# Optimization experiments

Measured on AMD Instinct MI355X. Metric: run time of the kernel, lower is better.

Reference implementation:

```python
import jax, jax.numpy as jnp
import numpy as np

B, F = 512, 300  # F must satisfy F+4 == 16*19
EPS = 1e-5

def _leaky(v):
    return jnp.where(v >= 0, v, 0.01 * v)

def setup_inputs() -> dict:
    key = jax.random.key(0)
    ks = jax.random.split(key, 9)
    def conv_w(k, o, i):
        return jax.random.normal(k, (o, i), dtype=jnp.float32) * (1.0 / np.sqrt(i))
    x = jax.random.uniform(ks[0], (B, F), dtype=jnp.float32)
    return {
        "x": x,
        "w1": conv_w(ks[1], 256, 512), "b1": jnp.zeros((256,), jnp.float32),
        "w2": conv_w(ks[2], 128, 256), "b2": jnp.zeros((128,), jnp.float32),
        "w3": conv_w(ks[3], 64, 128),  "b3": jnp.zeros((64,), jnp.float32),
        "w4": conv_w(ks[4], 4, 64),    "b4": jnp.zeros((4,), jnp.float32),
    }

def reference(x, w1, b1, w2, b2, w3, b3, w4, b4):
    b = x.shape[0]
    xp = jnp.pad(x, ((0, 0), (2, 2)))                       # (b, 304)
    s1 = xp[:, None, :]                                      # unsqueeze(1)
    s2 = xp[:, :, None]                                      # unsqueeze(2)
    DI = s1 - s2                                             # (b,304,304)
    NDI = DI / (s1 + s2 + EPS)
    t = jnp.stack([DI, NDI], axis=-1)                        # (b,304,304,2)
    # tile into 16x16 grid of 19x19 patches, concat patches along channel
    # channel c = (row*16+col)*2 + d  (row-major loop order in original)
    t = t.reshape(b, 16, 19, 16, 19, 2).transpose(0, 2, 4, 1, 3, 5).reshape(b, 19, 19, 512)
    h = _leaky(jnp.einsum('bhwc,oc->bhwo', t, w1) + b1)      # (b,19,19,256)
    h = _leaky(jnp.einsum('bhwc,oc->bhwo', h, w2) + b2)      # (b,19,19,128)
    # masking branch (positional encoding in original is dead code / overwritten)
    m = jax.nn.relu(jnp.einsum('bhwc,oc->bhwo', h, w3) + b3)  # (b,19,19,64)
    m = jax.nn.relu(jnp.einsum('bhwc,oc->bhwo', m, w4) + b4)  # (b,19,19,4)
    m = m.transpose(3, 0, 1, 2).reshape(4, b, 19 * 19)
    m = jax.nn.softmax(m, axis=2).reshape(4, b, 19, 19, 1)
    # split 128 channels into 4 groups of 32
    g = h.reshape(b, 19, 19, 4, 32).transpose(3, 0, 1, 2, 4)  # (4,b,19,19,32)
    out = (g * m).sum(axis=(2, 3))                            # (4,b,32)
    return out.transpose(1, 0, 2).reshape(b, 128)
```

## Files before the change

### kernel.cpp

```cpp
#include <hip/hip_runtime.h>
#include <math.h>

typedef unsigned short ushort_t;
typedef __attribute__((ext_vector_type(8))) short short8;
typedef __attribute__((ext_vector_type(4))) float f32x4;

#define NTILES 12

#define WS_W_USHORTS 115712

__device__ inline float bf2f(ushort_t h) { return __uint_as_float(((unsigned)h) << 16); }
__device__ inline ushort_t f2bf(float f) {
    unsigned u = __float_as_uint(f);
    return (ushort_t)((u + 0x7FFFu + ((u >> 16) & 1u)) >> 16);
}
__device__ inline unsigned pkbf(float f0, float f1) {
    unsigned a = __float_as_uint(f0) + 0x8000u;
    unsigned b = __float_as_uint(f1) + 0x8000u;
    return __builtin_amdgcn_perm(b, a, 0x07060302u);
}
__device__ inline float leaky(float v) { return v >= 0.f ? v : 0.01f * v; }

__global__ void pack_weights(const float* __restrict__ w1, const float* __restrict__ w2,
                             const float* __restrict__ w3, const float* __restrict__ w4,
                             ushort_t* __restrict__ ws) {
    const int idx = blockIdx.x * 256 + threadIdx.x;
    if (idx >= WS_W_USHORTS) return;
    float val = 0.f;
    if (idx < 73728) {
        const int j = idx & 7, lane = (idx >> 3) & 63, blk = idx >> 9;
        const int ks = blk % 9, os = blk / 9;
        const int m = lane & 15, q = lane >> 4;
        const int row = os * 16 + m;
        if (ks < 8) {
            const int k = ks * 32 + q * 8 + j;
            const int i1 = k >> 4, j1 = k & 15;
            val = w1[row * 512 + i1 * 32 + j1 * 2 + 1];
        } else {
            const int sub = q * 8 + j;
            if (sub < 16) {
                const int j1 = sub;
                float s = 0.f;
                #pragma unroll
                for (int i1 = 0; i1 < 16; ++i1) s += w1[row * 512 + i1 * 32 + j1 * 2];
                val = s;
            } else {
                const int i1 = sub - 16;
                float s = 0.f;
                #pragma unroll
                for (int j1 = 0; j1 < 16; ++j1) s += w1[row * 512 + i1 * 32 + j1 * 2];
                val = -s;
            }
        }
    } else if (idx < 106496) {
        const int l = idx - 73728;
        const int j = l & 7, lane = (l >> 3) & 63, blk = l >> 9;
        const int ks = blk & 7, os = blk >> 3;
        const int m = lane & 15, q = lane >> 4;
        val = w2[(os * 16 + m) * 256 + ks * 32 + q * 8 + j];
    } else if (idx < 114688) {
        const int l = idx - 106496;
        const int j = l & 7, lane = (l >> 3) & 63, blk = l >> 9;
        const int ks = blk & 3, os = blk >> 2;
        const int m = lane & 15, q = lane >> 4;
        val = w3[(os * 16 + m) * 128 + ks * 32 + q * 8 + j];
    } else {
        const int l = idx - 114688;
        const int j = l & 7, lane = (l >> 3) & 63, ks = l >> 9;
        const int m = lane & 15, q = lane >> 4;
        val = (m < 4) ? w4[m * 64 + ks * 32 + q * 8 + j] : 0.f;
    }
    ws[idx] = f2bf(val);
}

template <int NS>
__global__ __launch_bounds__(256, 3) void fused_mfma(
    const float* __restrict__ x, const ushort_t* __restrict__ ws,
    const float* __restrict__ b1, const float* __restrict__ b2,
    const float* __restrict__ b3, const float* __restrict__ b4,
    float* __restrict__ part)
{
    __shared__ __align__(16) ushort_t sm[23144];
    ushort_t* const ts  = sm;
    ushort_t* const h1s = sm + 10240;
    ushort_t* const h2s = sm + 18432;
    ushort_t* const m3s = sm + 10240;
    float*   const lgs  = (float*)(sm + 12288);
    float*   const xp   = (float*)(sm + 22528);

    constexpr int SH  = (NS == 4) ? 2 : ((NS == 2) ? 1 : 0);
    constexpr int TPS = (NTILES + NS - 1) / NS;
    const int tid = threadIdx.x;
    const int s   = blockIdx.x & (NS - 1);
    const int bb  = blockIdx.x >> SH;
    const int t0  = s * TPS;
    const int t1  = (t0 + TPS < NTILES) ? (t0 + TPS) : NTILES;

    const int wid  = tid >> 6;
    const int lane = tid & 63;
    const int n0   = lane & 15;
    const int qi   = lane >> 4;
    const int sx   = n0 & 7;
    const int row0 = qi * 4;

    for (int jj = tid; jj < 308; jj += 256) {
        float v = 0.f;
        const int src = jj - 2;
        if (src >= 0 && src < 300) v = x[bb * 300 + src];
        xp[jj] = v;
    }
    __syncthreads();

    const short8* wf1 = (const short8*)(ws);
    const short8* wf2 = (const short8*)(ws + 73728);
    const short8* wf3 = (const short8*)(ws + 106496);
    const short8* wf4 = (const short8*)(ws + 114688);

    const int qh   = (tid >> 5) & 3;
    const int ch   = tid & 127;
    const int half = tid >> 7;
    float M = -1e30f, S = 0.f, A = 0.f;
    const f32x4 z4 = {0.f, 0.f, 0.f, 0.f};

    for (int tile = t0; tile < t1; ++tile) {
        const int pos0 = tile * 32;

        {
            const int p   = tid & 31;
            const int i1b = tid >> 5;
            int posg = pos0 + p; if (posg > 360) posg = 360;
            const int hh = posg / 19;
            const int ww = posg - 19 * hh;
            const int base = p * 320;
            const int psw  = p & 7;
            float u[16];
            #pragma unroll
            for (int j1 = 0; j1 < 16; ++j1) u[j1] = xp[j1 * 19 + ww];
            #pragma unroll
            for (int ii = 0; ii < 2; ++ii) {
                const int i1 = i1b + ii * 8;
                const float v = xp[i1 * 19 + hh];
                #pragma unroll
                for (int j1 = 0; j1 < 16; j1 += 2) {
                    const float nd0 = (u[j1] - v)     * __builtin_amdgcn_rcpf(u[j1] + v + 1e-5f);
                    const float nd1 = (u[j1 + 1] - v) * __builtin_amdgcn_rcpf(u[j1 + 1] + v + 1e-5f);
                    const int oct = i1 * 2 + (j1 >> 3);
                    *(unsigned*)&ts[base + ((oct ^ psw) << 3) + (j1 & 7)] = pkbf(nd0, nd1);
                }
            }
            if (i1b == 0) {
                #pragma unroll
                for (int j1 = 0; j1 < 16; j1 += 2) {
                    const int oct = 32 + (j1 >> 3);
                    *(unsigned*)&ts[base + ((oct ^ psw) << 3) + (j1 & 7)] = pkbf(u[j1], u[j1 + 1]);
                }
                #pragma unroll
                for (int i1 = 0; i1 < 16; i1 += 2) {
                    const float v0 = xp[i1 * 19 + hh];
                    const float v1 = xp[(i1 + 1) * 19 + hh];
                    const int oct = 34 + (i1 >> 3);
                    *(unsigned*)&ts[base + ((oct ^ psw) << 3) + (i1 & 7)] = pkbf(v0, v1);
                }
            }
        }
        __syncthreads();

        {
            f32x4 acc[4][2];
            #pragma unroll
            for (int jo = 0; jo < 4; ++jo) { acc[jo][0] = z4; acc[jo][1] = z4; }
            const int tb0 = n0 * 320;
            const int tb1 = tb0 + 16 * 320;
            const int wbase = wid * 2304 + lane;
            #pragma unroll 3
            for (int ks = 0; ks < 9; ++ks) {
                const int oct = ks * 4 + qi;
                const short8 bb0 = *(const short8*)&ts[tb0 + ((oct ^ sx) << 3)];
                const short8 bb1 = *(const short8*)&ts[tb1 + ((oct ^ sx) << 3)];
                #pragma unroll
                for (int jo = 0; jo < 4; ++jo) {
                    const short8 a = wf1[wbase + (jo * 9 + ks) * 64];
                    acc[jo][0] = __builtin_amdgcn_mfma_f32_16x16x32_bf16(a, bb0, acc[jo][0], 0, 0, 0);
                    acc[jo][1] = __builtin_amdgcn_mfma_f32_16x16x32_bf16(a, bb1, acc[jo][1], 0, 0, 0);
                }
            }
            #pragma unroll
            for (int jo = 0; jo < 4; ++jo) {
                const int out0 = (wid * 4 + jo) * 16 + row0;
                const f32x4 bv = *(const f32x4*)&b1[out0];
                #pragma unroll
                for (int ps = 0; ps < 2; ++ps) {
                    const f32x4 a4 = acc[jo][ps];
                    uint2 pk;
                    pk.x = pkbf(leaky(a4.x + bv.x), leaky(a4.y + bv.y));
                    pk.y = pkbf(leaky(a4.z + bv.z), leaky(a4.w + bv.w));
                    *(uint2*)&h1s[(ps * 16 + n0) * 256 + (((out0 >> 3) ^ sx) << 3) + (out0 & 7)] = pk;
                }
            }
        }
        __syncthreads();

        {
            f32x4 acc[2][2];
            #pragma unroll
            for (int jo = 0; jo < 2; ++jo) { acc[jo][0] = z4; acc[jo][1] = z4; }
            const int hb0 = n0 * 256;
            const int hb1 = hb0 + 16 * 256;
            const int wbase = wid * 1024 + lane;
            #pragma unroll 4
            for (int ks = 0; ks < 8; ++ks) {
                const int oct = ks * 4 + qi;
                const short8 bb0 = *(const short8*)&h1s[hb0 + ((oct ^ sx) << 3)];
                const short8 bb1 = *(const short8*)&h1s[hb1 + ((oct ^ sx) << 3)];
                #pragma unroll
                for (int jo = 0; jo < 2; ++jo) {
                    const short8 a = wf2[wbase + (jo * 8 + ks) * 64];
                    acc[jo][0] = __builtin_amdgcn_mfma_f32_16x16x32_bf16(a, bb0, acc[jo][0], 0, 0, 0);
                    acc[jo][1] = __builtin_amdgcn_mfma_f32_16x16x32_bf16(a, bb1, acc[jo][1], 0, 0, 0);
                }
            }
            #pragma unroll
            for (int jo = 0; jo < 2; ++jo) {
                const int out0 = (wid * 2 + jo) * 16 + row0;
                const f32x4 bv = *(const f32x4*)&b2[out0];
                #pragma unroll
                for (int ps = 0; ps < 2; ++ps) {
                    const f32x4 a4 = acc[jo][ps];
                    uint2 pk;
                    pk.x = pkbf(leaky(a4.x + bv.x), leaky(a4.y + bv.y));
                    pk.y = pkbf(leaky(a4.z + bv.z), leaky(a4.w + bv.w));
                    *(uint2*)&h2s[(ps * 16 + n0) * 128 + (((out0 >> 3) ^ sx) << 3) + (out0 & 7)] = pk;
                }
            }
        }
        __syncthreads();

        {
            f32x4 acc[2] = {z4, z4};
            const int cb0 = n0 * 128;
            const int cb1 = cb0 + 16 * 128;
            #pragma unroll
            for (int ks = 0; ks < 4; ++ks) {
                const int oct = ks * 4 + qi;
                const short8 bb0 = *(const short8*)&h2s[cb0 + ((oct ^ sx) << 3)];
                const short8 bb1 = *(const short8*)&h2s[cb1 + ((oct ^ sx) << 3)];
                const short8 a = wf3[(wid * 4 + ks) * 64 + lane];
                acc[0] = __builtin_amdgcn_mfma_f32_16x16x32_bf16(a, bb0, acc[0], 0, 0, 0);
                acc[1] = __builtin_amdgcn_mfma_f32_16x16x32_bf16(a, bb1, acc[1], 0, 0, 0);
            }
            const int out0 = wid * 16 + row0;
            const f32x4 bv = *(const f32x4*)&b3[out0];
            #pragma unroll
            for (int ps = 0; ps < 2; ++ps) {
                const f32x4 a4 = acc[ps];
                uint2 pk;
                pk.x = pkbf(fmaxf(a4.x + bv.x, 0.f), fmaxf(a4.y + bv.y, 0.f));
                pk.y = pkbf(fmaxf(a4.z + bv.z, 0.f), fmaxf(a4.w + bv.w, 0.f));
                *(uint2*)&m3s[(ps * 16 + n0) * 64 + (((out0 >> 3) ^ sx) << 3) + (out0 & 7)] = pk;
            }
        }
        __syncthreads();

        if (wid == 0) {
            f32x4 acc[2] = {z4, z4};
            const int mb0 = n0 * 64;
            const int mb1 = mb0 + 16 * 64;
            #pragma unroll
            for (int ks = 0; ks < 2; ++ks) {
                const int oct = ks * 4 + qi;
                const short8 bb0 = *(const short8*)&m3s[mb0 + ((oct ^ sx) << 3)];
                const short8 bb1 = *(const short8*)&m3s[mb1 + ((oct ^ sx) << 3)];
                const short8 a = wf4[ks * 64 + lane];
                acc[0] = __builtin_amdgcn_mfma_f32_16x16x32_bf16(a, bb0, acc[0], 0, 0, 0);
                acc[1] = __builtin_amdgcn_mfma_f32_16x16x32_bf16(a, bb1, acc[1], 0, 0, 0);
            }
            if (lane < 16) {
                const f32x4 bv = *(const f32x4*)&b4[0];
                #pragma unroll
                for (int ps = 0; ps < 2; ++ps) {
                    const int pos = ps * 16 + lane;
                    const bool bad = (pos0 + pos) > 360;
                    const f32x4 a4 = acc[ps];
                    lgs[0 * 32 + pos] = bad ? -1e30f : fmaxf(a4.x + bv.x, 0.f);
                    lgs[1 * 32 + pos] = bad ? -1e30f : fmaxf(a4.y + bv.y, 0.f);
                    lgs[2 * 32 + pos] = bad ? -1e30f : fmaxf(a4.z + bv.z, 0.f);
                    lgs[3 * 32 + pos] = bad ? -1e30f : fmaxf(a4.w + bv.w, 0.f);
                }
            }
        }
        __syncthreads();

        {
            float l[16];
            float tmax = -1e30f;
            #pragma unroll
            for (int p8 = 0; p8 < 16; ++p8) {
                l[p8] = lgs[qh * 32 + half * 16 + p8];
                tmax = fmaxf(tmax, l[p8]);
            }
            const float newM  = fmaxf(M, tmax);
            const float alpha = __expf(M - newM);
            float ssum = 0.f, asum = 0.f;
            const int oc = ch >> 3, el = ch & 7;
            #pragma unroll
            for (int p8 = 0; p8 < 16; ++p8) {
                const int p = half * 16 + p8;
                const float ev = __expf(l[p8] - newM);
                ssum += ev;
                asum += ev * bf2f(h2s[p * 128 + ((oc ^ (p & 7)) << 3) + el]);
            }
            S = S * alpha + ssum;
            A = A * alpha + asum;
            M = newM;
        }
    }

    float* mbuf = (float*)ts;
    if (half == 1) {
        mbuf[ch] = M; mbuf[128 + ch] = S; mbuf[256 + ch] = A;
    }
    __syncthreads();
    if (half == 0) {
        const float M1 = mbuf[ch], S1 = mbuf[128 + ch], A1 = mbuf[256 + ch];
        const float Mf = fmaxf(M, M1);
        const float e0 = __expf(M - Mf), e1 = __expf(M1 - Mf);
        const int pb  = (s * 512 + bb) * 128 + ch;
        const int sep = NS * 512 * 128;
        part[pb]           = Mf;
        part[pb + sep]     = S * e0 + S1 * e1;
        part[pb + 2 * sep] = A * e0 + A1 * e1;
    }
}

template <int NS>
__global__ void merge_out(const float* __restrict__ part, float* __restrict__ out) {
    const int idx = blockIdx.x * 256 + threadIdx.x;
    if (idx >= 512 * 128) return;
    const int bb = idx >> 7, ch = idx & 127;
    const int sep = NS * 512 * 128;
    float Mf = -1e30f;
    #pragma unroll
    for (int s = 0; s < NS; ++s) Mf = fmaxf(Mf, part[(s * 512 + bb) * 128 + ch]);
    float Sf = 0.f, Af = 0.f;
    #pragma unroll
    for (int s = 0; s < NS; ++s) {
        const int pb = (s * 512 + bb) * 128 + ch;
        const float e = __expf(part[pb] - Mf);
        Sf += part[pb + sep] * e;
        Af += part[pb + 2 * sep] * e;
    }
    out[idx] = Af / Sf;
}

__global__ __launch_bounds__(256, 2) void fallback_fused(
    const float* __restrict__ x,
    const float* __restrict__ w1, const float* __restrict__ b1,
    const float* __restrict__ w2, const float* __restrict__ b2,
    const float* __restrict__ w3, const float* __restrict__ b3,
    const float* __restrict__ w4, const float* __restrict__ b4,
    float* __restrict__ out)
{
    __shared__ float smf[14644];
    float* const xp  = smf;
    float* const ts  = smf + 308;
    float* const h1s = smf + 8500;
    float* const h2s = smf + 12596;
    float* const m3s = ts;
    float* const lgs = ts + 1024;

    const int tid = threadIdx.x;
    const int b   = blockIdx.x;
    for (int j = tid; j < 308; j += 256) {
        float v = 0.f;
        const int src = j - 2;
        if (src >= 0 && src < 300) v = x[b * 300 + src];
        xp[j] = v;
    }
    __syncthreads();
    const int q = tid >> 5, dd = tid & 31;
    float M = -1e30f, S = 0.f, A = 0.f;
    for (int tile = 0; tile < 23; ++tile) {
        const int pos0 = tile * 16;
        {
            const int p = tid & 15, kk0 = tid >> 4;
            const int pos = pos0 + p;
            const bool valid = (pos < 361);
            const int hh = valid ? (pos / 19) : 0;
            const int ww = valid ? (pos - hh * 19) : 0;
            #pragma unroll
            for (int i = 0; i < 16; ++i) {
                const int kk = kk0 + (i << 4);
                const int i1 = kk >> 4, j1 = kk & 15;
                float di = 0.f, ndi = 0.f;
                if (valid) {
                    const float u = xp[j1 * 19 + ww];
                    const float v = xp[i1 * 19 + hh];
                    di = u - v; ndi = di / (u + v + 1e-5f);
                }
                ts[(kk << 5) + p] = di;
                ts[(kk << 5) + 16 + p] = ndi;
            }
        }
        __syncthreads();
        {
            const int o = tid;
            float acc[16];
            const float bias = b1[o];
            #pragma unroll
            for (int p = 0; p < 16; ++p) acc[p] = bias;
            for (int k = 0; k < 512; ++k) {
                const float wv = w1[o * 512 + k];
                #pragma unroll
                for (int p = 0; p < 16; ++p) acc[p] += wv * ts[(k << 4) + p];
            }
            #pragma unroll
            for (int p = 0; p < 16; ++p) h1s[(o << 4) + p] = leaky(acc[p]);
        }
        __syncthreads();
        {
            const int o2 = tid & 127, pb = (tid >> 7) << 3;
            float acc[8];
            const float bias = b2[o2];
            #pragma unroll
            for (int j = 0; j < 8; ++j) acc[j] = bias;
            for (int k = 0; k < 256; ++k) {
                const float wv = w2[o2 * 256 + k];
                #pragma unroll
                for (int j = 0; j < 8; ++j) acc[j] += wv * h1s[(k << 4) + pb + j];
            }
            #pragma unroll
            for (int j = 0; j < 8; ++j) h2s[(o2 << 4) + pb + j] = leaky(acc[j]);
        }
        __syncthreads();
        {
            const int o3 = tid & 63, pb = (tid >> 6) << 2;
            float acc[4];
            const float bias = b3[o3];
            #pragma unroll
            for (int j = 0; j < 4; ++j) acc[j] = bias;
            for (int k = 0; k < 128; ++k) {
                const float wv = w3[o3 * 128 + k];
                #pragma unroll
                for (int j = 0; j < 4; ++j) acc[j] += wv * h2s[(k << 4) + pb + j];
            }
            #pragma unroll
            for (int j = 0; j < 4; ++j) m3s[(o3 << 4) + pb + j] = fmaxf(acc[j], 0.f);
        }
        __syncthreads();
        if (tid < 64) {
            const int o4 = tid >> 4, p = tid & 15;
            float a = b4[o4];
            for (int k = 0; k < 64; ++k) a += w4[o4 * 64 + k] * m3s[(k << 4) + p];
            a = fmaxf(a, 0.f);
            if (pos0 + p >= 361) a = -1e30f;
            lgs[(o4 << 4) + p] = a;
        }
        __syncthreads();
        if (tid < 128) {
            float l[16];
            #pragma unroll
            for (int p = 0; p < 16; ++p) l[p] = lgs[(q << 4) + p];
            float tmax = l[0];
            #pragma unroll
            for (int p = 1; p < 16; ++p) tmax = fmaxf(tmax, l[p]);
            const float newM = fmaxf(M, tmax);
            const float alpha = __expf(M - newM);
            float ssum = 0.f, asum = 0.f;
            #pragma unroll
            for (int p = 0; p < 16; ++p) {
                const float e = __expf(l[p] - newM);
                ssum += e;
                asum += e * h2s[(((q << 5) + dd) << 4) + p];
            }
            S = S * alpha + ssum; A = A * alpha + asum; M = newM;
        }
        __syncthreads();
    }
    if (tid < 128) out[(b << 7) + tid] = A / S;
}

extern "C" void kernel_launch(void* const* d_in, const int* in_sizes, int n_in,
                              void* d_out, int out_size, void* d_ws, size_t ws_size,
                              hipStream_t stream) {
    const float* x  = (const float*)d_in[0];
    const float* w1 = (const float*)d_in[1];
    const float* b1 = (const float*)d_in[2];
    const float* w2 = (const float*)d_in[3];
    const float* b2 = (const float*)d_in[4];
    const float* w3 = (const float*)d_in[5];
    const float* b3 = (const float*)d_in[6];
    const float* w4 = (const float*)d_in[7];
    const float* b4 = (const float*)d_in[8];
    float* out = (float*)d_out;

    const size_t wbytes  = (size_t)WS_W_USHORTS * sizeof(ushort_t);
    const size_t pbytes1 = (size_t)3 * 512 * 128 * sizeof(float);
    ushort_t* ws = (ushort_t*)d_ws;
    float* partf = (float*)((char*)d_ws + wbytes);

    const int packBlocks = (WS_W_USHORTS + 255) / 256;
    if (ws_size >= wbytes + 4 * pbytes1) {
        pack_weights<<<packBlocks, 256, 0, stream>>>(w1, w2, w3, w4, ws);
        fused_mfma<4><<<2048, 256, 0, stream>>>(x, ws, b1, b2, b3, b4, partf);
        merge_out<4><<<256, 256, 0, stream>>>(partf, out);
    } else if (ws_size >= wbytes + 2 * pbytes1) {
        pack_weights<<<packBlocks, 256, 0, stream>>>(w1, w2, w3, w4, ws);
        fused_mfma<2><<<1024, 256, 0, stream>>>(x, ws, b1, b2, b3, b4, partf);
        merge_out<2><<<256, 256, 0, stream>>>(partf, out);
    } else if (ws_size >= wbytes + pbytes1) {
        pack_weights<<<packBlocks, 256, 0, stream>>>(w1, w2, w3, w4, ws);
        fused_mfma<1><<<512, 256, 0, stream>>>(x, ws, b1, b2, b3, b4, partf);
        merge_out<1><<<256, 256, 0, stream>>>(partf, out);
    } else {
        fallback_fused<<<512, 256, 0, stream>>>(x, w1, b1, w2, b2, w3, b3, w4, b4, out);
    }
}
```

Before: 164.9 us.

## Shrink shared memory, preload biases, fuse softmax into MFMA epilogue with shuffles

Reduces the LDS footprint by aliasing h2s onto the input tile buffer, which adds an extra barrier after layer 1 so the buffer can be reused. Biases are loaded once into registers and used as the MFMA accumulator initial value instead of being added per tile. The online-softmax max and exp are now computed in wave 0 with cross-lane shuffles, and the weighted accumulation is spread across all 256 threads, each handling two channels and an 8-position slice. Leaky ReLU becomes a single fmax. The aim is higher occupancy and less per-tile softmax work, at the cost of one more sync per tile and a longer serial step in wave 0.

```diff
diff --git a/kernel.cpp b/kernel.cpp
--- a/kernel.cpp
+++ b/kernel.cpp
@@ -19,7 +19,7 @@
     unsigned b = __float_as_uint(f1) + 0x8000u;
     return __builtin_amdgcn_perm(b, a, 0x07060302u);
 }
-__device__ inline float leaky(float v) { return v >= 0.f ? v : 0.01f * v; }
+__device__ inline float leaky(float v) { return fmaxf(v, 0.01f * v); }
 
 __global__ void pack_weights(const float* __restrict__ w1, const float* __restrict__ w2,
                              const float* __restrict__ w3, const float* __restrict__ w4,
@@ -80,13 +80,14 @@
     const float* __restrict__ b3, const float* __restrict__ b4,
     float* __restrict__ part)
 {
-    __shared__ __align__(16) ushort_t sm[23144];
-    ushort_t* const ts  = sm;
-    ushort_t* const h1s = sm + 10240;
-    ushort_t* const h2s = sm + 18432;
-    ushort_t* const m3s = sm + 10240;
-    float*   const lgs  = (float*)(sm + 12288);
-    float*   const xp   = (float*)(sm + 22528);
+    __shared__ __align__(16) ushort_t sm[19048];
+    ushort_t* const ts   = sm;
+    ushort_t* const h2s  = sm;
+    ushort_t* const h1s  = sm + 10240;
+    ushort_t* const m3s  = sm + 10240;
+    float*   const ebuf  = (float*)(sm + 12288);
+    float*   const abuf  = (float*)(sm + 12544);
+    float*   const xp    = (float*)(sm + 18432);
 
     constexpr int SH  = (NS == 4) ? 2 : ((NS == 2) ? 1 : 0);
     constexpr int TPS = (NTILES + NS - 1) / NS;
@@ -109,18 +110,27 @@
         if (src >= 0 && src < 300) v = x[bb * 300 + src];
         xp[jj] = v;
     }
-    __syncthreads();
 
     const short8* wf1 = (const short8*)(ws);
     const short8* wf2 = (const short8*)(ws + 73728);
     const short8* wf3 = (const short8*)(ws + 106496);
     const short8* wf4 = (const short8*)(ws + 114688);
 
-    const int qh   = (tid >> 5) & 3;
-    const int ch   = tid & 127;
-    const int half = tid >> 7;
-    float M = -1e30f, S = 0.f, A = 0.f;
-    const f32x4 z4 = {0.f, 0.f, 0.f, 0.f};
+    f32x4 bv1[4], bv2[2], bv3, bv4;
+    #pragma unroll
+    for (int jo = 0; jo < 4; ++jo) bv1[jo] = *(const f32x4*)&b1[(wid * 4 + jo) * 16 + row0];
+    #pragma unroll
+    for (int jo = 0; jo < 2; ++jo) bv2[jo] = *(const f32x4*)&b2[(wid * 2 + jo) * 16 + row0];
+    bv3 = *(const f32x4*)&b3[wid * 16 + row0];
+    bv4 = *(const f32x4*)&b4[0];
+
+    const int cp = tid & 63;
+    const int qt = tid >> 6;
+    const int qq = cp >> 4;
+    float A0 = 0.f, A1 = 0.f, Ss = 0.f;
+    float Mq[4] = {-1e30f, -1e30f, -1e30f, -1e30f};
+
+    __syncthreads();
 
     for (int tile = t0; tile < t1; ++tile) {
         const int pos0 = tile * 32;
@@ -165,10 +175,10 @@
         }
         __syncthreads();
 
-        {
-            f32x4 acc[4][2];
-            #pragma unroll
-            for (int jo = 0; jo < 4; ++jo) { acc[jo][0] = z4; acc[jo][1] = z4; }
+        f32x4 acc1[4][2];
+        {
+            #pragma unroll
+            for (int jo = 0; jo < 4; ++jo) { acc1[jo][0] = bv1[jo]; acc1[jo][1] = bv1[jo]; }
             const int tb0 = n0 * 320;
             const int tb1 = tb0 + 16 * 320;
             const int wbase = wid * 2304 + lane;
@@ -180,20 +190,22 @@
                 #pragma unroll
                 for (int jo = 0; jo < 4; ++jo) {
                     const short8 a = wf1[wbase + (jo * 9 + ks) * 64];
-                    acc[jo][0] = __builtin_amdgcn_mfma_f32_16x16x32_bf16(a, bb0, acc[jo][0], 0, 0, 0);
-                    acc[jo][1] = __builtin_amdgcn_mfma_f32_16x16x32_bf16(a, bb1, acc[jo][1], 0, 0, 0);
-                }
-            }
+                    acc1[jo][0] = __builtin_amdgcn_mfma_f32_16x16x32_bf16(a, bb0, acc1[jo][0], 0, 0, 0);
+                    acc1[jo][1] = __builtin_amdgcn_mfma_f32_16x16x32_bf16(a, bb1, acc1[jo][1], 0, 0, 0);
+                }
+            }
+        }
+        __syncthreads();
+        {
             #pragma unroll
             for (int jo = 0; jo < 4; ++jo) {
                 const int out0 = (wid * 4 + jo) * 16 + row0;
-                const f32x4 bv = *(const f32x4*)&b1[out0];
                 #pragma unroll
                 for (int ps = 0; ps < 2; ++ps) {
-                    const f32x4 a4 = acc[jo][ps];
+                    const f32x4 a4 = acc1[jo][ps];
                     uint2 pk;
-                    pk.x = pkbf(leaky(a4.x + bv.x), leaky(a4.y + bv.y));
-                    pk.y = pkbf(leaky(a4.z + bv.z), leaky(a4.w + bv.w));
+                    pk.x = pkbf(leaky(a4.x), leaky(a4.y));
+                    pk.y = pkbf(leaky(a4.z), leaky(a4.w));
                     *(uint2*)&h1s[(ps * 16 + n0) * 256 + (((out0 >> 3) ^ sx) << 3) + (out0 & 7)] = pk;
                 }
             }
@@ -203,7 +215,7 @@
         {
             f32x4 acc[2][2];
             #pragma unroll
-            for (int jo = 0; jo < 2; ++jo) { acc[jo][0] = z4; acc[jo][1] = z4; }
+            for (int jo = 0; jo < 2; ++jo) { acc[jo][0] = bv2[jo]; acc[jo][1] = bv2[jo]; }
             const int hb0 = n0 * 256;
             const int hb1 = hb0 + 16 * 256;
             const int wbase = wid * 1024 + lane;
@@ -222,13 +234,12 @@
             #pragma unroll
             for (int jo = 0; jo < 2; ++jo) {
                 const int out0 = (wid * 2 + jo) * 16 + row0;
-                const f32x4 bv = *(const f32x4*)&b2[out0];
                 #pragma unroll
                 for (int ps = 0; ps < 2; ++ps) {
                     const f32x4 a4 = acc[jo][ps];
                     uint2 pk;
-                    pk.x = pkbf(leaky(a4.x + bv.x), leaky(a4.y + bv.y));
-                    pk.y = pkbf(leaky(a4.z + bv.z), leaky(a4.w + bv.w));
+                    pk.x = pkbf(leaky(a4.x), leaky(a4.y));
+                    pk.y = pkbf(leaky(a4.z), leaky(a4.w));
                     *(uint2*)&h2s[(ps * 16 + n0) * 128 + (((out0 >> 3) ^ sx) << 3) + (out0 & 7)] = pk;
                 }
             }
@@ -236,7 +247,7 @@
         __syncthreads();
 
         {
-            f32x4 acc[2] = {z4, z4};
+            f32x4 acc[2] = {bv3, bv3};
             const int cb0 = n0 * 128;
             const int cb1 = cb0 + 16 * 128;
             #pragma unroll
@@ -249,20 +260,19 @@
                 acc[1] = __builtin_amdgcn_mfma_f32_16x16x32_bf16(a, bb1, acc[1], 0, 0, 0);
             }
             const int out0 = wid * 16 + row0;
-            const f32x4 bv = *(const f32x4*)&b3[out0];
             #pragma unroll
             for (int ps = 0; ps < 2; ++ps) {
                 const f32x4 a4 = acc[ps];
                 uint2 pk;
-                pk.x = pkbf(fmaxf(a4.x + bv.x, 0.f), fmaxf(a4.y + bv.y, 0.f));
-                pk.y = pkbf(fmaxf(a4.z + bv.z, 0.f), fmaxf(a4.w + bv.w, 0.f));
+                pk.x = pkbf(fmaxf(a4.x, 0.f), fmaxf(a4.y, 0.f));
+                pk.y = pkbf(fmaxf(a4.z, 0.f), fmaxf(a4.w, 0.f));
                 *(uint2*)&m3s[(ps * 16 + n0) * 64 + (((out0 >> 3) ^ sx) << 3) + (out0 & 7)] = pk;
             }
         }
         __syncthreads();
 
         if (wid == 0) {
-            f32x4 acc[2] = {z4, z4};
+            f32x4 acc[2] = {bv4, bv4};
             const int mb0 = n0 * 64;
             const int mb1 = mb0 + 16 * 64;
             #pragma unroll
@@ -274,61 +284,78 @@
                 acc[0] = __builtin_amdgcn_mfma_f32_16x16x32_bf16(a, bb0, acc[0], 0, 0, 0);
                 acc[1] = __builtin_amdgcn_mfma_f32_16x16x32_bf16(a, bb1, acc[1], 0, 0, 0);
             }
-            if (lane < 16) {
-                const f32x4 bv = *(const f32x4*)&b4[0];
-                #pragma unroll
-                for (int ps = 0; ps < 2; ++ps) {
-                    const int pos = ps * 16 + lane;
-                    const bool bad = (pos0 + pos) > 360;
-                    const f32x4 a4 = acc[ps];
-                    lgs[0 * 32 + pos] = bad ? -1e30f : fmaxf(a4.x + bv.x, 0.f);
-                    lgs[1 * 32 + pos] = bad ? -1e30f : fmaxf(a4.y + bv.y, 0.f);
-                    lgs[2 * 32 + pos] = bad ? -1e30f : fmaxf(a4.z + bv.z, 0.f);
-                    lgs[3 * 32 + pos] = bad ? -1e30f : fmaxf(a4.w + bv.w, 0.f);
-                }
-            }
-        }
-        __syncthreads();
-
-        {
-            float l[16];
-            float tmax = -1e30f;
-            #pragma unroll
-            for (int p8 = 0; p8 < 16; ++p8) {
-                l[p8] = lgs[qh * 32 + half * 16 + p8];
-                tmax = fmaxf(tmax, l[p8]);
-            }
-            const float newM  = fmaxf(M, tmax);
-            const float alpha = __expf(M - newM);
-            float ssum = 0.f, asum = 0.f;
-            const int oc = ch >> 3, el = ch & 7;
-            #pragma unroll
-            for (int p8 = 0; p8 < 16; ++p8) {
-                const int p = half * 16 + p8;
-                const float ev = __expf(l[p8] - newM);
-                ssum += ev;
-                asum += ev * bf2f(h2s[p * 128 + ((oc ^ (p & 7)) << 3) + el]);
-            }
-            S = S * alpha + ssum;
-            A = A * alpha + asum;
-            M = newM;
-        }
-    }
-
-    float* mbuf = (float*)ts;
-    if (half == 1) {
-        mbuf[ch] = M; mbuf[128 + ch] = S; mbuf[256 + ch] = A;
-    }
+            const bool bad0 = (pos0 + lane) > 360;
+            const bool bad1 = (pos0 + 16 + lane) > 360;
+            float l0[4], l1[4];
+            l0[0] = bad0 ? -1e30f : fmaxf(acc[0].x, 0.f);
+            l0[1] = bad0 ? -1e30f : fmaxf(acc[0].y, 0.f);
+            l0[2] = bad0 ? -1e30f : fmaxf(acc[0].z, 0.f);
+            l0[3] = bad0 ? -1e30f : fmaxf(acc[0].w, 0.f);
+            l1[0] = bad1 ? -1e30f : fmaxf(acc[1].x, 0.f);
+            l1[1] = bad1 ? -1e30f : fmaxf(acc[1].y, 0.f);
+            l1[2] = bad1 ? -1e30f : fmaxf(acc[1].z, 0.f);
+            l1[3] = bad1 ? -1e30f : fmaxf(acc[1].w, 0.f);
+            #pragma unroll
+            for (int q = 0; q < 4; ++q) {
+                float tm = fmaxf(l0[q], l1[q]);
+                tm = fmaxf(tm, __shfl_xor(tm, 1, 64));
+                tm = fmaxf(tm, __shfl_xor(tm, 2, 64));
+                tm = fmaxf(tm, __shfl_xor(tm, 4, 64));
+                tm = fmaxf(tm, __shfl_xor(tm, 8, 64));
+                const float nM = fmaxf(Mq[q], tm);
+                const float al = __expf(Mq[q] - nM);
+                Mq[q] = nM;
+                const float e0 = __expf(l0[q] - nM);
+                const float e1 = __expf(l1[q] - nM);
+                if (lane < 16) {
+                    ebuf[q * 32 + lane]      = e0;
+                    ebuf[q * 32 + 16 + lane] = e1;
+                }
+                if (lane == 0) abuf[q] = al;
+            }
+        }
+        __syncthreads();
+
+        {
+            const float alpha = abuf[qq];
+            A0 *= alpha; A1 *= alpha; Ss *= alpha;
+            const int oc4 = cp >> 2;
+            const int elo = (cp & 3) * 2;
+            #pragma unroll
+            for (int pp = 0; pp < 8; ++pp) {
+                const int p = qt * 8 + pp;
+                const float e = ebuf[qq * 32 + p];
+                const unsigned hp = *(const unsigned*)&h2s[p * 128 + ((oc4 ^ (p & 7)) << 3) + elo];
+                const float f0 = __uint_as_float(hp << 16);
+                const float f1 = __uint_as_float(hp & 0xFFFF0000u);
+                A0 += e * f0;
+                A1 += e * f1;
+                Ss += e;
+            }
+        }
+        __syncthreads();
+    }
+
+    float* mbuf = (float*)(sm + 10240);
+    mbuf[qt * 64 + cp]        = A0;
+    mbuf[256 + qt * 64 + cp]  = A1;
+    mbuf[512 + qt * 64 + cp]  = Ss;
+    if (wid == 0 && lane < 4) mbuf[768 + lane] = Mq[lane];
     __syncthreads();
-    if (half == 0) {
-        const float M1 = mbuf[ch], S1 = mbuf[128 + ch], A1 = mbuf[256 + ch];
-        const float Mf = fmaxf(M, M1);
-        const float e0 = __expf(M - Mf), e1 = __expf(M1 - Mf);
+    if (tid < 128) {
+        const int ch = tid, cpf = ch >> 1, par = ch & 1;
+        float Af = 0.f, Sf = 0.f;
+        #pragma unroll
+        for (int t = 0; t < 4; ++t) {
+            Af += mbuf[par * 256 + t * 64 + cpf];
+            Sf += mbuf[512 + t * 64 + cpf];
+        }
+        const float Mf = mbuf[768 + (ch >> 5)];
         const int pb  = (s * 512 + bb) * 128 + ch;
         const int sep = NS * 512 * 128;
         part[pb]           = Mf;
-        part[pb + sep]     = S * e0 + S1 * e1;
-        part[pb + 2 * sep] = A * e0 + A1 * e1;
+        part[pb + sep]     = Sf;
+        part[pb + 2 * sep] = Af;
     }
 }
 
@@ -414,7 +441,7 @@
                 for (int p = 0; p < 16; ++p) acc[p] += wv * ts[(k << 4) + p];
             }
             #pragma unroll
-            for (int p = 0; p < 16; ++p) h1s[(o << 4) + p] = leaky(acc[p]);
+            for (int p = 0; p < 16; ++p) h1s[(o << 4) + p] = (acc[p] >= 0.f) ? acc[p] : 0.01f * acc[p];
         }
         __syncthreads();
         {
@@ -429,7 +456,7 @@
                 for (int j = 0; j < 8; ++j) acc[j] += wv * h1s[(k << 4) + pb + j];
             }
             #pragma unroll
-            for (int j = 0; j < 8; ++j) h2s[(o2 << 4) + pb + j] = leaky(acc[j]);
+            for (int j = 0; j < 8; ++j) h2s[(o2 << 4) + pb + j] = (acc[j] >= 0.f) ? acc[j] : 0.01f * acc[j];
         }
         __syncthreads();
         {
```

Measured after the change: 176.0 us. 1.07x slower.
